# Optimization experiments

Measured on AMD Instinct MI355X. Metric: run time of the kernel, lower is better.

The kernel has to match this reference:

```python
import jax, jax.numpy as jnp
import numpy as np

B, N, IN_DIM = 2, 2048, 1024
HEADS, HEAD_DIM = 16, 64

def setup_inputs() -> dict:
    key = jax.random.key(0)
    k1, k2, k3, k4, k5 = jax.random.split(key, 5)
    s_in = 1.0 / np.sqrt(IN_DIM)
    s_h = 1.0 / np.sqrt(HEADS * HEAD_DIM)
    return {
        "x": jax.random.normal(k1, (B, N, IN_DIM), jnp.float32),
        "w_qkv": jax.random.normal(k2, (IN_DIM, 3 * HEADS * HEAD_DIM), jnp.float32) * s_in,
        "b_qkv": jax.random.normal(k3, (3 * HEADS * HEAD_DIM,), jnp.float32) * s_in,
        "w_proj": jax.random.normal(k4, (HEADS * HEAD_DIM, IN_DIM), jnp.float32) * s_h,
        "b_proj": jax.random.normal(k5, (IN_DIM,), jnp.float32) * s_h,
    }

def reference(x, w_qkv, b_qkv, w_proj, b_proj):
    b, n, _ = x.shape
    scale = HEAD_DIM ** (-0.5)
    qkv = x @ w_qkv + b_qkv                               # (B,N,3*H*D)
    # torch: reshape(B,N,H,3*D).permute(0,2,1,3) then chunk last dim into q,k,v
    qkv = qkv.reshape(b, n, HEADS, 3 * HEAD_DIM).transpose(0, 2, 1, 3)  # (B,H,N,3D)
    q, k, v = jnp.split(qkv, 3, axis=-1)                  # each (B,H,N,D)
    attn = jnp.einsum("bhqd,bhkd->bhqk", q, k) * scale    # (B,H,N,N)
    attn = jax.nn.softmax(attn, axis=-1)
    out = jnp.einsum("bhqk,bhkd->bhqd", attn, v)          # (B,H,N,D)
    out = out.transpose(0, 2, 1, 3).reshape(b, n, HEADS * HEAD_DIM)
    return out @ w_proj + b_proj
```

## Files before the change

kernel.cpp:

```cpp
#include <hip/hip_runtime.h>
#include <hip/hip_bf16.h>
#include <cstdint>
#include <cstddef>

#define BD 2
#define SEQ 2048
#define NH 16
#define HD 64
#define IND 1024
#define QKVD 3072
#define MROWS (BD * SEQ)
#define NSPLIT 2
#define TILES_PER_SPLIT (SEQ / 64 / NSPLIT)

typedef __attribute__((ext_vector_type(8))) short s8v;
typedef __attribute__((ext_vector_type(4))) short s4v;
typedef __attribute__((ext_vector_type(4))) float f4v;

__device__ __forceinline__ short f2bf(float f) {
  __hip_bfloat16 h = __float2bfloat16(f);
  return *reinterpret_cast<short*>(&h);
}

__device__ __forceinline__ float fexp2(float x) {
  float r;
  asm("v_exp_f32 %0, %1" : "=v"(r) : "v"(x));
  return r;
}

__device__ __forceinline__ void async_copy16(void* lds, const void* g) {
  __builtin_amdgcn_global_load_lds(
      (const __attribute__((address_space(1))) unsigned int*)g,
      (__attribute__((address_space(3))) unsigned int*)lds, 16, 0, 0);
}

__device__ __forceinline__ const s8v* lds_frag(const short* p, int row, int col) {
  int byte = (row << 7) + (col << 1);
  byte ^= ((row & 7) << 4);
  return (const s8v*)((const char*)p + byte);
}

__global__ void k_prep(const float* __restrict__ x, short* __restrict__ xb,
                       const float* __restrict__ w_qkv, short* __restrict__ wqT,
                       const float* __restrict__ w_proj, short* __restrict__ wpT) {
  __shared__ float tile[32][33];
  const int bid = blockIdx.x, t = threadIdx.x;
  if (bid < 4096) {
    const int i = bid * 256 + t;
    float4 v = reinterpret_cast<const float4*>(x)[i];
    s4v o;
    o[0] = f2bf(v.x); o[1] = f2bf(v.y); o[2] = f2bf(v.z); o[3] = f2bf(v.w);
    reinterpret_cast<s4v*>(xb)[i] = o;
    return;
  }
  const float* w; short* wT; int R, C, bx, by;
  if (bid < 4096 + 3072) {
    w = w_qkv; wT = wqT; R = IND; C = QKVD;
    const int tb = bid - 4096; bx = tb % 96; by = tb / 96;
  } else {
    w = w_proj; wT = wpT; R = IND; C = IND;
    const int tb = bid - 7168; bx = tb & 31; by = tb >> 5;
  }
  const int c0 = bx * 32, r0 = by * 32;
  const int tx = t & 31, ty = t >> 5;
  #pragma unroll
  for (int j = 0; j < 32; j += 8)
    tile[ty + j][tx] = w[(size_t)(r0 + ty + j) * C + c0 + tx];
  __syncthreads();
  #pragma unroll
  for (int j = 0; j < 32; j += 8)
    wT[(size_t)(c0 + ty + j) * R + r0 + tx] = f2bf(tile[tx][ty + j]);
}

template <int MODE>
__global__ __launch_bounds__(256) void k_gemm(const short* __restrict__ A,
                                              const short* __restrict__ BT,
                                              const float* __restrict__ bias,
                                              short* __restrict__ obf,
                                              float* __restrict__ ofl,
                                              int Mr, int Nc, int K) {
  constexpr int BM = 128, BN = 128, BK = 64;
  __shared__ short As[BM * BK];
  __shared__ short Bs[BN * BK];
  const int rm = blockIdx.x * BM, cn = blockIdx.y * BN;
  const int t = threadIdx.x, l = t & 63;
  const int wm = (t >> 6) >> 1, wn = (t >> 6) & 1;
  const int lr = l & 15, lc = l >> 4;

  int sRow[4], sCh[4];
  #pragma unroll
  for (int p = 0; p < 4; ++p) {
    const int c = p * 256 + t;
    sRow[p] = c >> 3;
    sCh[p] = ((c & 7) ^ (sRow[p] & 7)) * 8;
  }

  f4v acc[4][4];
  #pragma unroll
  for (int m = 0; m < 4; ++m)
    #pragma unroll
    for (int n = 0; n < 4; ++n) acc[m][n] = (f4v)0.0f;

  for (int k0 = 0; k0 < K; k0 += BK) {
    __syncthreads();
    #pragma unroll
    for (int p = 0; p < 4; ++p) {
      const int c = p * 256 + t;
      async_copy16((char*)As + c * 16, &A[(size_t)(rm + sRow[p]) * K + k0 + sCh[p]]);
      async_copy16((char*)Bs + c * 16, &BT[(size_t)(cn + sRow[p]) * K + k0 + sCh[p]]);
    }
    __syncthreads();
    #pragma unroll
    for (int ks = 0; ks < 2; ++ks) {
      s8v af[4], bf[4];
      #pragma unroll
      for (int m = 0; m < 4; ++m)
        af[m] = *lds_frag(As, wm * 64 + m * 16 + lr, ks * 32 + lc * 8);
      #pragma unroll
      for (int n = 0; n < 4; ++n)
        bf[n] = *lds_frag(Bs, wn * 64 + n * 16 + lr, ks * 32 + lc * 8);
      #pragma unroll
      for (int m = 0; m < 4; ++m)
        #pragma unroll
        for (int n = 0; n < 4; ++n)
          acc[m][n] = __builtin_amdgcn_mfma_f32_16x16x32_bf16(af[m], bf[n], acc[m][n], 0, 0, 0);
    }
  }

  const int row0 = rm + wm * 64, col0 = cn + wn * 64;
  #pragma unroll
  for (int n = 0; n < 4; ++n) {
    const int col = col0 + n * 16 + lr;
    const float bv = bias[col];
    if (MODE == 0) {
      const int h = col / 192, rem = col % 192;
      const int wch = rem >> 6, d = rem & 63;
      const float scale = (wch == 0) ? 0.125f * 1.44269504f : 1.0f;
      short* dst = obf + (size_t)wch * ((size_t)BD * NH * SEQ * HD);
      #pragma unroll
      for (int m = 0; m < 4; ++m)
        #pragma unroll
        for (int r = 0; r < 4; ++r) {
          const int row = row0 + m * 16 + lc * 4 + r;
          const int b = row >> 11, nn = row & (SEQ - 1);
          const short val = f2bf((acc[m][n][r] + bv) * scale);
          if (wch == 2)
            dst[((size_t)(b * NH + h) * HD + d) * SEQ + nn] = val;
          else
            dst[((size_t)(b * NH + h) * SEQ + nn) * HD + d] = val;
        }
    } else {
      #pragma unroll
      for (int m = 0; m < 4; ++m)
        #pragma unroll
        for (int r = 0; r < 4; ++r) {
          const int row = row0 + m * 16 + lc * 4 + r;
          ofl[(size_t)row * Nc + col] = acc[m][n][r] + bv;
        }
    }
  }
}

__global__ __launch_bounds__(256, 6) void k_attn(const short* __restrict__ Qw,
                                                 const short* __restrict__ Kw,
                                                 const short* __restrict__ Vt_g,
                                                 float* __restrict__ OP0,
                                                 float* __restrict__ OP1,
                                                 float* __restrict__ ML) {
  const int qb = blockIdx.x, bh = blockIdx.y, split = blockIdx.z;
  const size_t base = (size_t)bh * SEQ * HD;
  const int t = threadIdx.x, l = t & 63, w = t >> 6;
  const int lr = l & 15, lc = l >> 4;
  __shared__ short Ks[64 * 64];
  __shared__ short Vt[64 * 64];
  __shared__ short Ps[4][16 * 64];
  const int q0 = qb * 64 + w * 16;

  int ldsOff[2], kOff[2], vOff[2];
  #pragma unroll
  for (int p = 0; p < 2; ++p) {
    const int c = p * 256 + t;
    const int row = c >> 3, ch = (c & 7) ^ (row & 7);
    ldsOff[p] = c * 16;
    kOff[p] = row * HD + ch * 8;
    vOff[p] = row * SEQ + ch * 8;
  }
  const short* Kb = Kw + base;
  const short* Vb = Vt_g + base;

  s8v qf[2];
  #pragma unroll
  for (int s = 0; s < 2; ++s)
    qf[s] = *(const s8v*)&Qw[base + (size_t)(q0 + lr) * HD + s * 32 + lc * 8];

  f4v of[4];
  #pragma unroll
  for (int j = 0; j < 4; ++j) of[j] = (f4v)0.0f;
  float Mx = -3.0e38f, Ls = 0.0f;
  short* Pw = &Ps[w][0];

  for (int tt = 0; tt < TILES_PER_SPLIT; ++tt) {
    const size_t kv = (size_t)(split * TILES_PER_SPLIT + tt) * 64;
    __syncthreads();
    #pragma unroll
    for (int p = 0; p < 2; ++p)
      async_copy16((char*)Ks + ldsOff[p], Kb + kv * HD + kOff[p]);
    #pragma unroll
    for (int p = 0; p < 2; ++p)
      async_copy16((char*)Vt + ldsOff[p], Vb + kv + vOff[p]);
    __syncthreads();

    f4v st[4];
    #pragma unroll
    for (int j = 0; j < 4; ++j) st[j] = (f4v)0.0f;
    #pragma unroll
    for (int j = 0; j < 4; ++j)
      #pragma unroll
      for (int s = 0; s < 2; ++s) {
        s8v kf = *lds_frag(Ks, j * 16 + lr, s * 32 + lc * 8);
        st[j] = __builtin_amdgcn_mfma_f32_16x16x32_bf16(kf, qf[s], st[j], 0, 0, 0);
      }

    float mj[4];
    #pragma unroll
    for (int j = 0; j < 4; ++j)
      mj[j] = fmaxf(fmaxf(st[j][0], st[j][1]), fmaxf(st[j][2], st[j][3]));
    float pm = fmaxf(fmaxf(mj[0], mj[1]), fmaxf(mj[2], mj[3]));
    pm = fmaxf(pm, __shfl_xor(pm, 16));
    pm = fmaxf(pm, __shfl_xor(pm, 32));

    if (!__all(pm <= Mx + 8.0f)) {
      const float Mn = fmaxf(Mx, pm);
      const float alpha = fexp2(Mx - Mn);
      Ls *= alpha;
      float al[4];
      #pragma unroll
      for (int r = 0; r < 4; ++r) al[r] = __shfl(alpha, lc * 4 + r);
      #pragma unroll
      for (int jd = 0; jd < 4; ++jd)
        #pragma unroll
        for (int r = 0; r < 4; ++r) of[jd][r] *= al[r];
      Mx = Mn;
    }

    float rsj[4];
    #pragma unroll
    for (int j = 0; j < 4; ++j) {
      s4v pk;
      float pv[4];
      #pragma unroll
      for (int r = 0; r < 4; ++r) {
        pv[r] = fexp2(st[j][r] - Mx);
        pk[r] = f2bf(pv[r]);
      }
      rsj[j] = (pv[0] + pv[1]) + (pv[2] + pv[3]);
      int byte = (lr << 7) + ((j * 16 + lc * 4) << 1);
      byte ^= ((lr & 7) << 4);
      *(s4v*)((char*)Pw + byte) = pk;
    }
    float rs = (rsj[0] + rsj[1]) + (rsj[2] + rsj[3]);
    rs += __shfl_xor(rs, 16);
    rs += __shfl_xor(rs, 32);
    Ls += rs;

    asm volatile("s_waitcnt lgkmcnt(0)" ::: "memory");

    #pragma unroll
    for (int s = 0; s < 2; ++s) {
      s8v pf = *lds_frag(Pw, lr, s * 32 + lc * 8);
      #pragma unroll
      for (int jd = 0; jd < 4; ++jd) {
        s8v vf = *lds_frag(Vt, jd * 16 + lr, s * 32 + lc * 8);
        of[jd] = __builtin_amdgcn_mfma_f32_16x16x32_bf16(pf, vf, of[jd], 0, 0, 0);
      }
    }
  }

  float* OP = split ? OP1 : OP0;
  #pragma unroll
  for (int jd = 0; jd < 4; ++jd)
    #pragma unroll
    for (int r = 0; r < 4; ++r)
      OP[((size_t)bh * SEQ + q0 + lc * 4 + r) * HD + jd * 16 + lr] = of[jd][r];
  if (lc == 0) {
    float2 ml = make_float2(Mx, Ls);
    *reinterpret_cast<float2*>(
        &ML[((size_t)split * BD * NH * SEQ + (size_t)bh * SEQ + q0 + lr) * 2]) = ml;
  }
}

__global__ __launch_bounds__(256) void k_comb(const float* __restrict__ OP0,
                                              const float* __restrict__ OP1,
                                              const float* __restrict__ ML,
                                              short* __restrict__ AO) {
  const int gid = blockIdx.x * 256 + threadIdx.x;
  const int row = gid >> 2, c = gid & 3;
  const int bh = row >> 11, q = row & (SEQ - 1);
  const float2 ml1 = *reinterpret_cast<const float2*>(&ML[(size_t)row * 2]);
  const float2 ml2 = *reinterpret_cast<const float2*>(
      &ML[((size_t)BD * NH * SEQ + row) * 2]);
  const float M = fmaxf(ml1.x, ml2.x);
  const float w1 = fexp2(ml1.x - M), w2 = fexp2(ml2.x - M);
  const float inv = 1.0f / (w1 * ml1.y + w2 * ml2.y);
  const int b = bh >> 4, h = bh & 15;
  short* dst = &AO[((size_t)(b * SEQ + q) * (NH * HD)) + h * HD + c * 16];
  const size_t src = (size_t)row * HD + c * 16;
  #pragma unroll
  for (int i = 0; i < 4; ++i) {
    float4 a = reinterpret_cast<const float4*>(&OP0[src])[i];
    float4 bvv = reinterpret_cast<const float4*>(&OP1[src])[i];
    s4v o;
    o[0] = f2bf((w1 * a.x + w2 * bvv.x) * inv);
    o[1] = f2bf((w1 * a.y + w2 * bvv.y) * inv);
    o[2] = f2bf((w1 * a.z + w2 * bvv.z) * inv);
    o[3] = f2bf((w1 * a.w + w2 * bvv.w) * inv);
    reinterpret_cast<s4v*>(dst)[i] = o;
  }
}

extern "C" void kernel_launch(void* const* d_in, const int* in_sizes, int n_in,
                              void* d_out, int out_size, void* d_ws, size_t ws_size,
                              hipStream_t stream) {
  const float* x      = (const float*)d_in[0];
  const float* w_qkv  = (const float*)d_in[1];
  const float* b_qkv  = (const float*)d_in[2];
  const float* w_proj = (const float*)d_in[3];
  const float* b_proj = (const float*)d_in[4];
  float* out = (float*)d_out;

  char* ws = (char*)d_ws;
  short* wpT = (short*)(ws);
  short* Qw  = (short*)(ws + (2u << 20));
  short* Kw  = (short*)(ws + (10u << 20));
  short* Vtg = (short*)(ws + (18u << 20));
  short* AO  = (short*)(ws + (26u << 20));
  short* xb  = (short*)(ws + (34u << 20));
  short* wqT = (short*)(ws + (42u << 20));
  float* OP1 = (float*)(ws + (34u << 20));
  float* ML  = (float*)(ws + (50u << 20));
  float* OP0 = (float*)d_out;

  k_prep<<<4096 + 3072 + 1024, 256, 0, stream>>>(x, xb, w_qkv, wqT, w_proj, wpT);
  k_gemm<0><<<dim3(MROWS / 128, QKVD / 128), 256, 0, stream>>>(
      xb, wqT, b_qkv, Qw, nullptr, MROWS, QKVD, IND);
  k_attn<<<dim3(SEQ / 64, BD * NH, NSPLIT), 256, 0, stream>>>(Qw, Kw, Vtg, OP0, OP1, ML);
  k_comb<<<(BD * NH * SEQ * 4) / 256, 256, 0, stream>>>(OP0, OP1, ML, AO);
  k_gemm<1><<<dim3(MROWS / 128, IND / 128), 256, 0, stream>>>(
      AO, wpT, b_proj, nullptr, out, MROWS, IND, IND);
}
```

Measured before the change: 139.3 us.

## Feed softmax probabilities directly from registers into 16x16x16 MFMA for PV

```diff
diff --git a/kernel.cpp b/kernel.cpp
--- a/kernel.cpp
+++ b/kernel.cpp
@@ -161,7 +161,7 @@
   }
 }
 
-__global__ __launch_bounds__(256, 6) void k_attn(const short* __restrict__ Qw,
+__global__ __launch_bounds__(256, 8) void k_attn(const short* __restrict__ Qw,
                                                  const short* __restrict__ Kw,
                                                  const short* __restrict__ Vt_g,
                                                  float* __restrict__ OP0,
@@ -169,12 +169,11 @@
                                                  float* __restrict__ ML) {
   const int qb = blockIdx.x, bh = blockIdx.y, split = blockIdx.z;
   const size_t base = (size_t)bh * SEQ * HD;
-  const int t = threadIdx.x, l = t & 63, w = t >> 6;
+  const int t = threadIdx.x, l = t & 63;
   const int lr = l & 15, lc = l >> 4;
   __shared__ short Ks[64 * 64];
   __shared__ short Vt[64 * 64];
-  __shared__ short Ps[4][16 * 64];
-  const int q0 = qb * 64 + w * 16;
+  const int q0 = qb * 64 + (t >> 6) * 16;
 
   int ldsOff[2], kOff[2], vOff[2];
   #pragma unroll
@@ -193,11 +192,21 @@
   for (int s = 0; s < 2; ++s)
     qf[s] = *(const s8v*)&Qw[base + (size_t)(q0 + lr) * HD + s * 32 + lc * 8];
 
+  int vfOff[4][4];
+  #pragma unroll
+  for (int j = 0; j < 4; ++j)
+    #pragma unroll
+    for (int jd = 0; jd < 4; ++jd) {
+      const int row = jd * 16 + lr;
+      int byte = (row << 7) + ((j * 16 + lc * 4) << 1);
+      byte ^= ((row & 7) << 4);
+      vfOff[j][jd] = byte;
+    }
+
   f4v of[4];
   #pragma unroll
   for (int j = 0; j < 4; ++j) of[j] = (f4v)0.0f;
   float Mx = -3.0e38f, Ls = 0.0f;
-  short* Pw = &Ps[w][0];
 
   for (int tt = 0; tt < TILES_PER_SPLIT; ++tt) {
     const size_t kv = (size_t)(split * TILES_PER_SPLIT + tt) * 64;
@@ -243,38 +252,35 @@
       Mx = Mn;
     }
 
+    s4v pa[4];
     float rsj[4];
     #pragma unroll
     for (int j = 0; j < 4; ++j) {
-      s4v pk;
       float pv[4];
       #pragma unroll
       for (int r = 0; r < 4; ++r) {
         pv[r] = fexp2(st[j][r] - Mx);
-        pk[r] = f2bf(pv[r]);
+        pa[j][r] = f2bf(pv[r]);
       }
       rsj[j] = (pv[0] + pv[1]) + (pv[2] + pv[3]);
-      int byte = (lr << 7) + ((j * 16 + lc * 4) << 1);
-      byte ^= ((lr & 7) << 4);
-      *(s4v*)((char*)Pw + byte) = pk;
     }
     float rs = (rsj[0] + rsj[1]) + (rsj[2] + rsj[3]);
     rs += __shfl_xor(rs, 16);
     rs += __shfl_xor(rs, 32);
     Ls += rs;
 
-    asm volatile("s_waitcnt lgkmcnt(0)" ::: "memory");
-
-    #pragma unroll
-    for (int s = 0; s < 2; ++s) {
-      s8v pf = *lds_frag(Pw, lr, s * 32 + lc * 8);
+    #pragma unroll
+    for (int j = 0; j < 4; ++j) {
       #pragma unroll
       for (int jd = 0; jd < 4; ++jd) {
-        s8v vf = *lds_frag(Vt, jd * 16 + lr, s * 32 + lc * 8);
-        of[jd] = __builtin_amdgcn_mfma_f32_16x16x32_bf16(pf, vf, of[jd], 0, 0, 0);
+        s4v vf = *(const s4v*)((const char*)Vt + vfOff[j][jd]);
+        asm("v_mfma_f32_16x16x16_bf16 %0, %1, %2, %0"
+            : "+v"(of[jd]) : "v"(pa[j]), "v"(vf));
       }
     }
   }
+
+  asm volatile("s_nop 7\n\ts_nop 7");
 
   float* OP = split ? OP1 : OP0;
   #pragma unroll
```

Result: slower. 203.7 us (+46.2%).
